# Kernel optimization log

Measured on AMD Instinct MI355X. Metric: run time of the kernel, lower is better.

## Reference

```python
import jax, jax.numpy as jnp
import numpy as np

D, H, F, E, K = 1024, 16, 2048, 8, 2
EPS = 1e-5


def layernorm(x, g, b):
    m = jnp.mean(x, axis=-1, keepdims=True)
    v = jnp.mean((x - m) ** 2, axis=-1, keepdims=True)
    return (x - m) * jax.lax.rsqrt(v + EPS) * g + b


def mha(q_in, k_in, v_in, wq, wk, wv, bq, bk, bv, wo, bo):
    B, Tq, Dm = q_in.shape
    Tk = k_in.shape[1]
    dh = Dm // H
    q = (q_in @ wq + bq).reshape(B, Tq, H, dh)
    k = (k_in @ wk + bk).reshape(B, Tk, H, dh)
    v = (v_in @ wv + bv).reshape(B, Tk, H, dh)
    scores = jnp.einsum('bqhd,bkhd->bhqk', q, k) / jnp.sqrt(jnp.asarray(dh, q.dtype))
    attn = jax.nn.softmax(scores, axis=-1)
    out = jnp.einsum('bhqk,bkhd->bqhd', attn, v).reshape(B, Tq, Dm)
    return out @ wo + bo


def moe(x, rw, rb, w1, b1, w2, b2):
    B, T, Dm = x.shape
    xt = x.reshape(-1, Dm)                      # [N, D]
    N = xt.shape[0]
    logits = xt @ rw + rb                       # [N, E]
    probs = jax.nn.softmax(logits, axis=-1)
    topv, topi = jax.lax.top_k(probs, K)        # [N, K]
    gates = topv / jnp.sum(topv, axis=-1, keepdims=True)
    dense_gates = jnp.zeros((N, E), x.dtype).at[jnp.arange(N)[:, None], topi].set(gates)
    h = jax.nn.relu(jnp.einsum('td,edf->etf', xt, w1) + b1[:, None, :])  # [E, N, F]
    y = jnp.einsum('etf,efd->etd', h, w2) + b2[:, None, :]               # [E, N, D]
    out = jnp.einsum('te,etd->td', dense_gates, y).reshape(B, T, Dm)
    frac = jnp.mean(jnp.sum(jax.nn.one_hot(topi, E, dtype=x.dtype), axis=1) / K, axis=0)  # [E]
    importance = jnp.mean(probs, axis=0)        # [E]
    lb_loss = E * jnp.sum(frac * importance)
    return out, lb_loss


def forward(tgt, memory,
            sa_wq, sa_wk, sa_wv, sa_bq, sa_bk, sa_bv, sa_wo, sa_bo,
            ca_wq, ca_wk, ca_wv, ca_bq, ca_bk, ca_bv, ca_wo, ca_bo,
            ln1_g, ln1_b, ln2_g, ln2_b, ln3_g, ln3_b,
            rw, rb, w1, b1, w2, b2):
    t2 = mha(tgt, tgt, tgt, sa_wq, sa_wk, sa_wv, sa_bq, sa_bk, sa_bv, sa_wo, sa_bo)
    t = layernorm(tgt + t2, ln1_g, ln1_b)
    t2 = mha(t, memory, memory, ca_wq, ca_wk, ca_wv, ca_bq, ca_bk, ca_bv, ca_wo, ca_bo)
    t = layernorm(t + t2, ln2_g, ln2_b)
    t2, lb = moe(t, rw, rb, w1, b1, w2, b2)
    t = layernorm(t + t2, ln3_g, ln3_b)
    return t, lb


def setup_inputs() -> dict:
    key = jax.random.key(0)
    ks = jax.random.split(key, 24)
    s = 1.0 / np.sqrt(D)
    inp = {
        'tgt': jax.random.normal(ks[0], (4, 512, D), jnp.float32),
        'memory': jax.random.normal(ks[1], (4, 512, D), jnp.float32),
    }
    names = ['sa_wq', 'sa_wk', 'sa_wv', 'sa_wo', 'ca_wq', 'ca_wk', 'ca_wv', 'ca_wo']
    for i, n in enumerate(names):
        inp[n] = jax.random.normal(ks[2 + i], (D, D), jnp.float32) * s
    for n in ['sa_bq', 'sa_bk', 'sa_bv', 'sa_bo', 'ca_bq', 'ca_bk', 'ca_bv', 'ca_bo']:
        inp[n] = jnp.zeros((D,), jnp.float32)
    for n in ['ln1_g', 'ln2_g', 'ln3_g']:
        inp[n] = jnp.ones((D,), jnp.float32)
    for n in ['ln1_b', 'ln2_b', 'ln3_b']:
        inp[n] = jnp.zeros((D,), jnp.float32)
    inp['rw'] = jax.random.normal(ks[10], (D, E), jnp.float32) * s
    inp['rb'] = jnp.zeros((E,), jnp.float32)
    inp['w1'] = jax.random.normal(ks[11], (E, D, F), jnp.float32) * s
    inp['b1'] = jnp.zeros((E, F), jnp.float32)
    inp['w2'] = jax.random.normal(ks[12], (E, F, D), jnp.float32) * (1.0 / np.sqrt(F))
    inp['b2'] = jnp.zeros((E, D), jnp.float32)
    return inp


def reference(tgt, memory,
              sa_wq, sa_wk, sa_wv, sa_bq, sa_bk, sa_bv, sa_wo, sa_bo,
              ca_wq, ca_wk, ca_wv, ca_bq, ca_bk, ca_bv, ca_wo, ca_bo,
              ln1_g, ln1_b, ln2_g, ln2_b, ln3_g, ln3_b,
              rw, rb, w1, b1, w2, b2):
    return forward(tgt, memory,
                   sa_wq, sa_wk, sa_wv, sa_bq, sa_bk, sa_bv, sa_wo, sa_bo,
                   ca_wq, ca_wk, ca_wv, ca_bq, ca_bk, ca_bv, ca_wo, ca_bo,
                   ln1_g, ln1_b, ln2_g, ln2_b, ln3_g, ln3_b,
                   rw, rb, w1, b1, w2, b2)
```

## Files before the change

kernel.cpp:

```cpp
#include <hip/hip_runtime.h>

constexpr int Dm = 1024;
constexpr int NH = 16;
constexpr int Ff = 2048;
constexpr int NE = 8;
constexpr int Bn = 4;
constexpr int Tn = 512;
constexpr int Nt = 2048;

typedef float  f32x4  __attribute__((ext_vector_type(4)));
typedef __bf16 bf16x8 __attribute__((ext_vector_type(8)));
typedef unsigned short u16x8 __attribute__((ext_vector_type(8)));

__device__ inline unsigned short f2bf(float f) {
    unsigned u = __builtin_bit_cast(unsigned, f);
    u += 0x7FFFu + ((u >> 16) & 1u);
    return (unsigned short)(u >> 16);
}
__device__ inline float bf2f(unsigned short h) {
    unsigned u = (unsigned)h << 16;
    return __builtin_bit_cast(float, u);
}
__device__ inline void splitbf(float x, unsigned short& hi, unsigned short& lo) {
    hi = f2bf(x);
    lo = f2bf(x - bf2f(hi));
}
__device__ inline bf16x8 ld_frag(const unsigned short* p) {
    return __builtin_bit_cast(bf16x8, *(const u16x8*)p);
}

template <int SPLIT, int ABF, int CBF, int ACC>
__global__ __launch_bounds__(256) void gemm_bf16_kernel(
    const void* __restrict__ Ain, int lda,
    const float* __restrict__ W0, const float* __restrict__ W1,
    const float* __restrict__ W2, int ldw, size_t weStride,
    const float* __restrict__ B0, const float* __restrict__ B1,
    const float* __restrict__ B2, size_t beStride,
    void* __restrict__ Cout, int ldc,
    int Mparam, int K,
    const int* __restrict__ lst, int lstStride, const int* __restrict__ cnt,
    int mode, int relu,
    const void* __restrict__ Ain2, const float* __restrict__ W0b,
    const float* __restrict__ W1b, const float* __restrict__ B0b,
    const float* __restrict__ B1b, void* __restrict__ Cout2, int ldc2,
    int xSplit,
    const float* __restrict__ gatep, float* __restrict__ accOut)
{
    __shared__ __align__(16) unsigned short AsH[128 * 40];
    __shared__ __align__(16) unsigned short WsH[128 * 40];
    __shared__ __align__(16) unsigned short AsL[SPLIT ? 128 * 40 : 1];
    __shared__ __align__(16) unsigned short WsL[SPLIT ? 128 * 40 : 1];
    __shared__ int inIdx[128];
    __shared__ int outIdx[128];

    const int e = blockIdx.z;
    const int M = (mode == 0) ? Mparam : cnt[e];
    const int m0 = blockIdx.y * 128;
    if (m0 >= M) return;

    int bx = blockIdx.x;
    const void* Aptr = Ain;
    void* Cptr = Cout;
    int myldc = ldc;
    const float *w0 = W0, *w1 = W1, *w2 = W2, *b0 = B0, *b1 = B1, *b2 = B2;
    if (xSplit && bx >= xSplit) {
        bx -= xSplit;
        Aptr = Ain2; Cptr = Cout2; myldc = ldc2;
        w0 = W0b; w1 = W1b; w2 = W1b; b0 = B0b; b1 = B1b; b2 = B1b;
    }
    const int n0 = bx * 128;
    const int seg = n0 >> 10;
    const float* W = ((seg == 0) ? w0 : (seg == 1) ? w1 : w2) + (size_t)e * weStride;
    const float* bias = ((seg == 0) ? b0 : (seg == 1) ? b1 : b2) + (size_t)e * beStride;
    const int nseg = n0 & 1023;
    const int tid = threadIdx.x;

    if (tid < 128) {
        int g = m0 + tid;
        bool valid = g < M;
        int gi, go;
        if (mode == 0) { gi = valid ? g : (M - 1); go = valid ? g : -1; }
        else {
            int pid = lst[(size_t)e * lstStride + (valid ? g : 0)];
            gi = (mode == 1) ? (pid >> 1) : pid;
            go = valid ? pid : -1;
        }
        inIdx[tid] = gi;
        outIdx[tid] = go;
    }
    __syncthreads();

    const int ar = tid >> 1, ahalf = tid & 1;
    const int bn = (tid & 63) * 2, bko = ((tid >> 6) & 3) * 8;
    const float* aBaseF = ABF ? nullptr
        : ((const float*)Aptr + (size_t)inIdx[ar] * lda + ahalf * 16);
    const unsigned short* aBaseB = ABF
        ? ((const unsigned short*)Aptr + (size_t)inIdx[ar] * lda + ahalf * 16)
        : nullptr;
    const float* wBase = W + (size_t)bko * ldw + nseg + bn;

    const int lane = tid & 63, wv = tid >> 6;
    const int wy = (wv >> 1) * 64, wx = (wv & 1) * 64;
    const int l15 = lane & 15, quad = lane >> 4;

    f32x4 acc[4][4];
    #pragma unroll
    for (int i = 0; i < 4; ++i)
        #pragma unroll
        for (int j = 0; j < 4; ++j) acc[i][j] = (f32x4)0.f;

    float av[16];
    u16x8 a16[2];
    float2 wreg[8];

    auto loadA = [&](int k0) {
        if (ABF) {
            const unsigned short* ap = aBaseB + k0;
            a16[0] = *(const u16x8*)(ap);
            a16[1] = *(const u16x8*)(ap + 8);
        } else {
            const float* ap = aBaseF + k0;
            *(float4*)&av[0]  = *(const float4*)(ap);
            *(float4*)&av[4]  = *(const float4*)(ap + 4);
            *(float4*)&av[8]  = *(const float4*)(ap + 8);
            *(float4*)&av[12] = *(const float4*)(ap + 12);
        }
    };
    auto loadW = [&](int k0) {
        const float* wp = wBase + (size_t)k0 * ldw;
        #pragma unroll
        for (int j = 0; j < 8; ++j) wreg[j] = *(const float2*)(wp + (size_t)j * ldw);
    };
    auto storeA = [&]() {
        if (ABF) {
            *(u16x8*)&AsH[ar * 40 + ahalf * 16]     = a16[0];
            *(u16x8*)&AsH[ar * 40 + ahalf * 16 + 8] = a16[1];
        } else {
            u16x8 h0, h1, l0, l1;
            #pragma unroll
            for (int i = 0; i < 8; ++i) {
                if (SPLIT) {
                    unsigned short hh, ll;
                    splitbf(av[i], hh, ll); h0[i] = hh; l0[i] = ll;
                    splitbf(av[8 + i], hh, ll); h1[i] = hh; l1[i] = ll;
                } else {
                    h0[i] = f2bf(av[i]);
                    h1[i] = f2bf(av[8 + i]);
                }
            }
            *(u16x8*)&AsH[ar * 40 + ahalf * 16]     = h0;
            *(u16x8*)&AsH[ar * 40 + ahalf * 16 + 8] = h1;
            if (SPLIT) {
                *(u16x8*)&AsL[ar * 40 + ahalf * 16]     = l0;
                *(u16x8*)&AsL[ar * 40 + ahalf * 16 + 8] = l1;
            }
        }
    };
    auto storeW = [&]() {
        u16x8 h0, h1, l0, l1;
        #pragma unroll
        for (int j = 0; j < 8; ++j) {
            if (SPLIT) {
                unsigned short hh, ll;
                splitbf(wreg[j].x, hh, ll); h0[j] = hh; l0[j] = ll;
                splitbf(wreg[j].y, hh, ll); h1[j] = hh; l1[j] = ll;
            } else {
                h0[j] = f2bf(wreg[j].x);
                h1[j] = f2bf(wreg[j].y);
            }
        }
        *(u16x8*)&WsH[bn * 40 + bko]       = h0;
        *(u16x8*)&WsH[(bn + 1) * 40 + bko] = h1;
        if (SPLIT) {
            *(u16x8*)&WsL[bn * 40 + bko]       = l0;
            *(u16x8*)&WsL[(bn + 1) * 40 + bko] = l1;
        }
    };

    loadA(0);
    loadW(0);
    for (int k0 = 0; k0 < K; k0 += 32) {
        storeA();
        storeW();
        __syncthreads();
        if (k0 + 32 < K) { loadA(k0 + 32); loadW(k0 + 32); }
        bf16x8 ah[4], bh[4], al[4], bl[4];
        #pragma unroll
        for (int mi = 0; mi < 4; ++mi)
            ah[mi] = ld_frag(&AsH[(wy + mi * 16 + l15) * 40 + quad * 8]);
        #pragma unroll
        for (int ni = 0; ni < 4; ++ni)
            bh[ni] = ld_frag(&WsH[(wx + ni * 16 + l15) * 40 + quad * 8]);
        if (SPLIT) {
            #pragma unroll
            for (int mi = 0; mi < 4; ++mi)
                al[mi] = ld_frag(&AsL[(wy + mi * 16 + l15) * 40 + quad * 8]);
            #pragma unroll
            for (int ni = 0; ni < 4; ++ni)
                bl[ni] = ld_frag(&WsL[(wx + ni * 16 + l15) * 40 + quad * 8]);
        }
        #pragma unroll
        for (int mi = 0; mi < 4; ++mi)
            #pragma unroll
            for (int ni = 0; ni < 4; ++ni) {
                acc[mi][ni] = __builtin_amdgcn_mfma_f32_16x16x32_bf16(
                    ah[mi], bh[ni], acc[mi][ni], 0, 0, 0);
                if (SPLIT) {
                    acc[mi][ni] = __builtin_amdgcn_mfma_f32_16x16x32_bf16(
                        ah[mi], bl[ni], acc[mi][ni], 0, 0, 0);
                    acc[mi][ni] = __builtin_amdgcn_mfma_f32_16x16x32_bf16(
                        al[mi], bh[ni], acc[mi][ni], 0, 0, 0);
                }
            }
        __syncthreads();
    }

    #pragma unroll
    for (int mi = 0; mi < 4; ++mi) {
        #pragma unroll
        for (int r = 0; r < 4; ++r) {
            int rl = wy + mi * 16 + quad * 4 + r;
            int orow = outIdx[rl];
            if (orow < 0) continue;
            #pragma unroll
            for (int ni = 0; ni < 4; ++ni) {
                int col = n0 + wx + ni * 16 + l15;
                float val = acc[mi][ni][r] + bias[col & 1023];
                if (relu) val = fmaxf(val, 0.f);
                if (ACC) {
                    float g = gatep[orow];
                    atomicAdd(&accOut[(size_t)(orow >> 1) * Dm + col], g * val);
                } else if (CBF) {
                    ((unsigned short*)Cptr)[(size_t)orow * myldc + col] = f2bf(val);
                } else {
                    ((float*)Cptr)[(size_t)orow * myldc + col] = val;
                }
            }
        }
    }
}

__global__ __launch_bounds__(256) void attn_kernel(
    const float* __restrict__ Qp, int qld,
    const float* __restrict__ Kp, int kld, int kOff,
    const float* __restrict__ Vp, int vld, int vOff,
    float* __restrict__ O)
{
    __shared__ __align__(16) unsigned short KtH[64 * 72], KtL[64 * 72];
    __shared__ __align__(16) unsigned short VtH[64 * 72], VtL[64 * 72];
    __shared__ __align__(16) unsigned short PtH[4][16 * 72], PtL[4][16 * 72];

    const int tid = threadIdx.x, lane = tid & 63, wv = tid >> 6;
    const int quad = lane >> 4, l15 = lane & 15;
    const int b = blockIdx.z, h = blockIdx.y, q0 = blockIdx.x * 64;
    const int bT = b * Tn;

    bf16x8 aqh[2], aql[2];
    {
        const float* qp = Qp + (size_t)(bT + q0 + wv * 16 + l15) * qld + h * 64;
        #pragma unroll
        for (int s = 0; s < 2; ++s) {
            float v[8];
            *(float4*)&v[0] = *(const float4*)(qp + s * 32 + quad * 8);
            *(float4*)&v[4] = *(const float4*)(qp + s * 32 + quad * 8 + 4);
            u16x8 th, tl;
            #pragma unroll
            for (int i = 0; i < 8; ++i) {
                unsigned short hh, ll;
                splitbf(v[i], hh, ll); th[i] = hh; tl[i] = ll;
            }
            aqh[s] = __builtin_bit_cast(bf16x8, th);
            aql[s] = __builtin_bit_cast(bf16x8, tl);
        }
    }

    f32x4 oacc[4];
    #pragma unroll
    for (int i = 0; i < 4; ++i) oacc[i] = (f32x4)0.f;
    float mrow[4] = {-1e30f, -1e30f, -1e30f, -1e30f};
    float lrow[4] = {0.f, 0.f, 0.f, 0.f};

    const int rr = tid >> 2, cc = tid & 3;

    float kf[16], vf[16];
    auto loadKV = [&](int kt0) {
        const float* kr = Kp + (size_t)(bT + kt0 + rr) * kld + kOff + h * 64 + cc * 16;
        *(float4*)&kf[0]  = *(const float4*)(kr);
        *(float4*)&kf[4]  = *(const float4*)(kr + 4);
        *(float4*)&kf[8]  = *(const float4*)(kr + 8);
        *(float4*)&kf[12] = *(const float4*)(kr + 12);
        const float* vr = Vp + (size_t)(bT + kt0 + rr) * vld + vOff + h * 64 + cc * 16;
        *(float4*)&vf[0]  = *(const float4*)(vr);
        *(float4*)&vf[4]  = *(const float4*)(vr + 4);
        *(float4*)&vf[8]  = *(const float4*)(vr + 8);
        *(float4*)&vf[12] = *(const float4*)(vr + 12);
    };
    auto storeKV = [&]() {
        u16x8 h0, h1, l0, l1;
        #pragma unroll
        for (int i = 0; i < 8; ++i) {
            unsigned short hh, ll;
            splitbf(kf[i], hh, ll); h0[i] = hh; l0[i] = ll;
            splitbf(kf[8 + i], hh, ll); h1[i] = hh; l1[i] = ll;
        }
        *(u16x8*)&KtH[rr * 72 + cc * 16]     = h0;
        *(u16x8*)&KtH[rr * 72 + cc * 16 + 8] = h1;
        *(u16x8*)&KtL[rr * 72 + cc * 16]     = l0;
        *(u16x8*)&KtL[rr * 72 + cc * 16 + 8] = l1;
        #pragma unroll
        for (int i = 0; i < 16; ++i) {
            unsigned short hh, ll;
            splitbf(vf[i], hh, ll);
            VtH[(cc * 16 + i) * 72 + rr] = hh;
            VtL[(cc * 16 + i) * 72 + rr] = ll;
        }
    };

    loadKV(0);
    for (int kt0 = 0; kt0 < Tn; kt0 += 64) {
        storeKV();
        __syncthreads();
        if (kt0 + 64 < Tn) loadKV(kt0 + 64);

        f32x4 sacc[4];
        #pragma unroll
        for (int nt = 0; nt < 4; ++nt) {
            sacc[nt] = (f32x4)0.f;
            #pragma unroll
            for (int s = 0; s < 2; ++s) {
                bf16x8 bkh = ld_frag(&KtH[(nt * 16 + l15) * 72 + s * 32 + quad * 8]);
                bf16x8 bkl = ld_frag(&KtL[(nt * 16 + l15) * 72 + s * 32 + quad * 8]);
                sacc[nt] = __builtin_amdgcn_mfma_f32_16x16x32_bf16(aqh[s], bkh, sacc[nt], 0, 0, 0);
                sacc[nt] = __builtin_amdgcn_mfma_f32_16x16x32_bf16(aqh[s], bkl, sacc[nt], 0, 0, 0);
                sacc[nt] = __builtin_amdgcn_mfma_f32_16x16x32_bf16(aql[s], bkh, sacc[nt], 0, 0, 0);
            }
        }
        #pragma unroll
        for (int nt = 0; nt < 4; ++nt)
            #pragma unroll
            for (int r = 0; r < 4; ++r) sacc[nt][r] *= 0.125f;

        float alpha[4], mnew[4];
        #pragma unroll
        for (int r = 0; r < 4; ++r) {
            float mx = fmaxf(fmaxf(sacc[0][r], sacc[1][r]), fmaxf(sacc[2][r], sacc[3][r]));
            #pragma unroll
            for (int msk = 1; msk < 16; msk <<= 1) mx = fmaxf(mx, __shfl_xor(mx, msk));
            mnew[r] = fmaxf(mrow[r], mx);
            alpha[r] = __expf(mrow[r] - mnew[r]);
            mrow[r] = mnew[r];
        }
        float rs[4] = {0.f, 0.f, 0.f, 0.f};
        #pragma unroll
        for (int nt = 0; nt < 4; ++nt)
            #pragma unroll
            for (int r = 0; r < 4; ++r) {
                float p = __expf(sacc[nt][r] - mnew[r]);
                sacc[nt][r] = p;
                rs[r] += p;
            }
        #pragma unroll
        for (int r = 0; r < 4; ++r) {
            #pragma unroll
            for (int msk = 1; msk < 16; msk <<= 1) rs[r] += __shfl_xor(rs[r], msk);
            lrow[r] = lrow[r] * alpha[r] + rs[r];
        }
        #pragma unroll
        for (int ni = 0; ni < 4; ++ni)
            #pragma unroll
            for (int r = 0; r < 4; ++r) oacc[ni][r] *= alpha[r];

        #pragma unroll
        for (int nt = 0; nt < 4; ++nt)
            #pragma unroll
            for (int r = 0; r < 4; ++r) {
                unsigned short hh, ll;
                splitbf(sacc[nt][r], hh, ll);
                PtH[wv][(quad * 4 + r) * 72 + nt * 16 + l15] = hh;
                PtL[wv][(quad * 4 + r) * 72 + nt * 16 + l15] = ll;
            }
        asm volatile("s_waitcnt lgkmcnt(0)" ::: "memory");

        #pragma unroll
        for (int s = 0; s < 2; ++s) {
            bf16x8 aph = ld_frag(&PtH[wv][l15 * 72 + s * 32 + quad * 8]);
            bf16x8 apl = ld_frag(&PtL[wv][l15 * 72 + s * 32 + quad * 8]);
            #pragma unroll
            for (int ni = 0; ni < 4; ++ni) {
                bf16x8 bvh = ld_frag(&VtH[(ni * 16 + l15) * 72 + s * 32 + quad * 8]);
                bf16x8 bvl = ld_frag(&VtL[(ni * 16 + l15) * 72 + s * 32 + quad * 8]);
                oacc[ni] = __builtin_amdgcn_mfma_f32_16x16x32_bf16(aph, bvh, oacc[ni], 0, 0, 0);
                oacc[ni] = __builtin_amdgcn_mfma_f32_16x16x32_bf16(aph, bvl, oacc[ni], 0, 0, 0);
                oacc[ni] = __builtin_amdgcn_mfma_f32_16x16x32_bf16(apl, bvh, oacc[ni], 0, 0, 0);
            }
        }
        __syncthreads();
    }

    #pragma unroll
    for (int r = 0; r < 4; ++r) {
        float inv = 1.f / lrow[r];
        int orow = bT + q0 + wv * 16 + quad * 4 + r;
        #pragma unroll
        for (int ni = 0; ni < 4; ++ni) {
            int col = h * 64 + ni * 16 + l15;
            O[(size_t)orow * Dm + col] = oacc[ni][r] * inv;
        }
    }
}

__global__ __launch_bounds__(256) void ln_residual_kernel(
    const float* __restrict__ X, const float* __restrict__ R,
    const float* __restrict__ g, const float* __restrict__ bta,
    float* __restrict__ Out)
{
    __shared__ float red[8];
    const int t = blockIdx.x, tid = threadIdx.x;
    float v[4];
    float s = 0.f;
    #pragma unroll
    for (int i = 0; i < 4; ++i) {
        int c = tid + i * 256;
        v[i] = X[(size_t)t * Dm + c] + R[(size_t)t * Dm + c];
        s += v[i];
    }
    #pragma unroll
    for (int off = 32; off; off >>= 1) s += __shfl_down(s, off);
    const int wid = tid >> 6;
    if ((tid & 63) == 0) red[wid] = s;
    __syncthreads();
    const float mean = (red[0] + red[1] + red[2] + red[3]) * (1.f / 1024.f);
    float s2 = 0.f;
    #pragma unroll
    for (int i = 0; i < 4; ++i) { float d = v[i] - mean; s2 += d * d; }
    #pragma unroll
    for (int off = 32; off; off >>= 1) s2 += __shfl_down(s2, off);
    if ((tid & 63) == 0) red[4 + wid] = s2;
    __syncthreads();
    const float var  = (red[4] + red[5] + red[6] + red[7]) * (1.f / 1024.f);
    const float rstd = rsqrtf(var + 1e-5f);
    #pragma unroll
    for (int i = 0; i < 4; ++i) {
        int c = tid + i * 256;
        Out[(size_t)t * Dm + c] = (v[i] - mean) * rstd * g[c] + bta[c];
    }
}

constexpr int RT_TPB = 32;
__global__ __launch_bounds__(256) void router_kernel(
    const float* __restrict__ X, const float* __restrict__ rw,
    const float* __restrict__ rb, float* __restrict__ gatep,
    int* __restrict__ elist, int* __restrict__ ecnt,
    float* __restrict__ impf, float* __restrict__ cntf)
{
    __shared__ float simp[NE];
    __shared__ int   scnt[NE];
    __shared__ int   sbase[NE];
    __shared__ int   sexp[RT_TPB][2];
    __shared__ int   spos[RT_TPB][2];

    const int tid = threadIdx.x, lane = tid & 63, wv = tid >> 6;
    if (tid < NE) { simp[tid] = 0.f; scnt[tid] = 0; }
    __syncthreads();

    const int t0 = blockIdx.x * RT_TPB;

    for (int i = 0; i < 8; ++i) {
        const int slot = wv * 8 + i;
        const int t = t0 + slot;
        float l[NE];
        #pragma unroll
        for (int e = 0; e < NE; ++e) l[e] = 0.f;
        #pragma unroll
        for (int j = 0; j < Dm / 64; ++j) {
            int d = lane + j * 64;
            float x = X[(size_t)t * Dm + d];
            #pragma unroll
            for (int e = 0; e < NE; ++e) l[e] += x * rw[d * NE + e];
        }
        #pragma unroll
        for (int e = 0; e < NE; ++e) {
            float vv = l[e];
            #pragma unroll
            for (int off = 32; off; off >>= 1) vv += __shfl_down(vv, off);
            l[e] = vv;
        }
        if (lane == 0) {
            float mx = -1e30f;
            #pragma unroll
            for (int e = 0; e < NE; ++e) { l[e] += rb[e]; mx = fmaxf(mx, l[e]); }
            float p[NE];
            float sum = 0.f;
            #pragma unroll
            for (int e = 0; e < NE; ++e) { p[e] = __expf(l[e] - mx); sum += p[e]; }
            const float inv = 1.f / sum;
            int e0 = 0, e1 = 0;
            float v0 = -1.f, v1 = -1.f;
            #pragma unroll
            for (int e = 0; e < NE; ++e) {
                float pe = p[e] * inv;
                atomicAdd(&simp[e], pe);
                if (pe > v0)      { v1 = v0; e1 = e0; v0 = pe; e0 = e; }
                else if (pe > v1) { v1 = pe; e1 = e; }
            }
            const float gs = 1.f / (v0 + v1);
            sexp[slot][0] = e0;
            sexp[slot][1] = e1;
            spos[slot][0] = atomicAdd(&scnt[e0], 1);
            spos[slot][1] = atomicAdd(&scnt[e1], 1);
            gatep[2 * t]     = v0 * gs;
            gatep[2 * t + 1] = v1 * gs;
        }
    }
    __syncthreads();

    if (tid < NE) {
        sbase[tid] = atomicAdd(&ecnt[tid], scnt[tid]);
        atomicAdd(&impf[tid], simp[tid]);
        atomicAdd(&cntf[tid], (float)scnt[tid]);
    }
    __syncthreads();

    if (tid < RT_TPB * 2) {
        const int slot = tid >> 1, k = tid & 1;
        const int e = sexp[slot][k];
        elist[e * Nt + sbase[e] + spos[slot][k]] = 2 * (t0 + slot) + k;
    }
}

__global__ __launch_bounds__(256) void zero_kernel(
    float* __restrict__ t2, int* __restrict__ ecnt,
    float* __restrict__ impf, float* __restrict__ cntf)
{
    int i = blockIdx.x * 256 + threadIdx.x;
    *(float4*)&t2[(size_t)i * 4] = make_float4(0.f, 0.f, 0.f, 0.f);
    if (blockIdx.x == 0 && threadIdx.x < NE) {
        ecnt[threadIdx.x] = 0;
        impf[threadIdx.x] = 0.f;
        cntf[threadIdx.x] = 0.f;
    }
}

__global__ void lb_kernel(const float* __restrict__ impf,
                          const float* __restrict__ cntf,
                          float* __restrict__ out)
{
    if (threadIdx.x == 0) {
        float s = 0.f;
        for (int e = 0; e < NE; ++e) s += cntf[e] * impf[e];
        out[0] = (float)NE * s / ((float)Nt * 2.f * (float)Nt);
    }
}

extern "C" void kernel_launch(void* const* d_in, const int* in_sizes, int n_in,
                              void* d_out, int out_size, void* d_ws, size_t ws_size,
                              hipStream_t stream)
{
    const float* tgt   = (const float*)d_in[0];
    const float* memry = (const float*)d_in[1];
    const float* sa_wq = (const float*)d_in[2];
    const float* sa_wk = (const float*)d_in[3];
    const float* sa_wv = (const float*)d_in[4];
    const float* sa_wo = (const float*)d_in[5];
    const float* ca_wq = (const float*)d_in[6];
    const float* ca_wk = (const float*)d_in[7];
    const float* ca_wv = (const float*)d_in[8];
    const float* ca_wo = (const float*)d_in[9];
    const float* sa_bq = (const float*)d_in[10];
    const float* sa_bk = (const float*)d_in[11];
    const float* sa_bv = (const float*)d_in[12];
    const float* sa_bo = (const float*)d_in[13];
    const float* ca_bq = (const float*)d_in[14];
    const float* ca_bk = (const float*)d_in[15];
    const float* ca_bv = (const float*)d_in[16];
    const float* ca_bo = (const float*)d_in[17];
    const float* ln1_g = (const float*)d_in[18];
    const float* ln2_g = (const float*)d_in[19];
    const float* ln3_g = (const float*)d_in[20];
    const float* ln1_b = (const float*)d_in[21];
    const float* ln2_b = (const float*)d_in[22];
    const float* ln3_b = (const float*)d_in[23];
    const float* rw    = (const float*)d_in[24];
    const float* rb    = (const float*)d_in[25];
    const float* w1    = (const float*)d_in[26];
    const float* b1    = (const float*)d_in[27];
    const float* w2    = (const float*)d_in[28];
    const float* b2    = (const float*)d_in[29];

    float* ws = (float*)d_ws;
    const size_t ND = (size_t)Nt * Dm;
    float* qkv  = ws;
    float* qc   = ws;
    unsigned short* hbuf16 = (unsigned short*)ws;
    float* attnO = ws + 3 * ND;
    float* t2   = ws + 4 * ND;
    float* tb   = ws + 5 * ND;
    float* kvc  = ws + 6 * ND;
    float* gatep = ws + 8 * ND;
    int*   elist = (int*)(gatep + 2 * Nt);
    int*   ecnt  = elist + NE * Nt;
    float* impf  = (float*)(ecnt + NE);
    float* cntf  = impf + NE;
    float* outp  = (float*)d_out;

    dim3 blk(256);
    dim3 attnGrid(Tn / 64, NH, Bn);

    gemm_bf16_kernel<1, 0, 0, 0><<<dim3(40, 16, 1), blk, 0, stream>>>(
        tgt, Dm, sa_wq, sa_wk, sa_wv, Dm, 0, sa_bq, sa_bk, sa_bv, 0,
        qkv, 3 * Dm, Nt, Dm, nullptr, 0, nullptr, 0, 0,
        memry, ca_wk, ca_wv, ca_bk, ca_bv, kvc, 2 * Dm, 24,
        nullptr, nullptr);
    attn_kernel<<<attnGrid, blk, 0, stream>>>(
        qkv, 3 * Dm, qkv, 3 * Dm, 1024, qkv, 3 * Dm, 2048, attnO);
    gemm_bf16_kernel<1, 0, 0, 0><<<dim3(8, 16, 1), blk, 0, stream>>>(
        attnO, Dm, sa_wo, sa_wo, sa_wo, Dm, 0, sa_bo, sa_bo, sa_bo, 0,
        t2, Dm, Nt, Dm, nullptr, 0, nullptr, 0, 0,
        nullptr, nullptr, nullptr, nullptr, nullptr, nullptr, 0, 0,
        nullptr, nullptr);
    ln_residual_kernel<<<Nt, blk, 0, stream>>>(tgt, t2, ln1_g, ln1_b, tb);

    gemm_bf16_kernel<1, 0, 0, 0><<<dim3(8, 16, 1), blk, 0, stream>>>(
        tb, Dm, ca_wq, ca_wq, ca_wq, Dm, 0, ca_bq, ca_bq, ca_bq, 0,
        qc, Dm, Nt, Dm, nullptr, 0, nullptr, 0, 0,
        nullptr, nullptr, nullptr, nullptr, nullptr, nullptr, 0, 0,
        nullptr, nullptr);
    attn_kernel<<<attnGrid, blk, 0, stream>>>(
        qc, Dm, kvc, 2 * Dm, 0, kvc, 2 * Dm, 1024, attnO);
    gemm_bf16_kernel<1, 0, 0, 0><<<dim3(8, 16, 1), blk, 0, stream>>>(
        attnO, Dm, ca_wo, ca_wo, ca_wo, Dm, 0, ca_bo, ca_bo, ca_bo, 0,
        t2, Dm, Nt, Dm, nullptr, 0, nullptr, 0, 0,
        nullptr, nullptr, nullptr, nullptr, nullptr, nullptr, 0, 0,
        nullptr, nullptr);
    ln_residual_kernel<<<Nt, blk, 0, stream>>>(tb, t2, ln2_g, ln2_b, tb);

    zero_kernel<<<(Nt * Dm) / 1024, blk, 0, stream>>>(t2, ecnt, impf, cntf);
    router_kernel<<<Nt / RT_TPB, blk, 0, stream>>>(tb, rw, rb, gatep, elist, ecnt, impf, cntf);
    gemm_bf16_kernel<0, 0, 1, 0><<<dim3(16, 16, 8), blk, 0, stream>>>(
        tb, Dm, w1, w1 + 1024, w1 + 1024, Ff, (size_t)Dm * Ff, b1, b1 + 1024, b1 + 1024, Ff,
        hbuf16, Ff, 0, Dm, elist, Nt, ecnt, 1, 1,
        nullptr, nullptr, nullptr, nullptr, nullptr, nullptr, 0, 0,
        nullptr, nullptr);
    gemm_bf16_kernel<0, 1, 0, 1><<<dim3(8, 16, 8), blk, 0, stream>>>(
        hbuf16, Ff, w2, w2, w2, Dm, (size_t)Ff * Dm, b2, b2, b2, Dm,
        nullptr, Dm, 0, Ff, elist, Nt, ecnt, 2, 0,
        nullptr, nullptr, nullptr, nullptr, nullptr, nullptr, 0, 0,
        gatep, t2);
    ln_residual_kernel<<<Nt, blk, 0, stream>>>(tb, t2, ln3_g, ln3_b, outp);
    lb_kernel<<<1, 64, 0, stream>>>(impf, cntf, outp + ND);
}
```

Before: 819.6 us.

## Halve GEMM M-tile to 64 and drop register prefetch in GEMM and attention

The GEMM block tile shrinks from 128 to 64 rows, with each wave now computing a 32x64 sub-tile, and grids double along y to give more blocks. The register double-buffering (load the next tile before the MFMA loop) is removed from both the GEMM and attention kernels, so loads go straight to shared memory each iteration. This lowers register and shared-memory use per block, which should raise occupancy and parallelism. The cost is less overlap between global loads and compute, and more weight-tile reloading across blocks.

```diff
diff --git a/kernel.cpp b/kernel.cpp
--- a/kernel.cpp
+++ b/kernel.cpp
@@ -46,16 +46,16 @@
     int xSplit,
     const float* __restrict__ gatep, float* __restrict__ accOut)
 {
-    __shared__ __align__(16) unsigned short AsH[128 * 40];
+    __shared__ __align__(16) unsigned short AsH[64 * 40];
     __shared__ __align__(16) unsigned short WsH[128 * 40];
-    __shared__ __align__(16) unsigned short AsL[SPLIT ? 128 * 40 : 1];
+    __shared__ __align__(16) unsigned short AsL[SPLIT ? 64 * 40 : 1];
     __shared__ __align__(16) unsigned short WsL[SPLIT ? 128 * 40 : 1];
-    __shared__ int inIdx[128];
-    __shared__ int outIdx[128];
+    __shared__ int inIdx[64];
+    __shared__ int outIdx[64];
 
     const int e = blockIdx.z;
     const int M = (mode == 0) ? Mparam : cnt[e];
-    const int m0 = blockIdx.y * 128;
+    const int m0 = blockIdx.y * 64;
     if (m0 >= M) return;
 
     int bx = blockIdx.x;
@@ -75,7 +75,7 @@
     const int nseg = n0 & 1023;
     const int tid = threadIdx.x;
 
-    if (tid < 128) {
+    if (tid < 64) {
         int g = m0 + tid;
         bool valid = g < M;
         int gi, go;
@@ -90,117 +90,89 @@
     }
     __syncthreads();
 
-    const int ar = tid >> 1, ahalf = tid & 1;
+    const int ar = tid >> 2, ahalf = tid & 3;
     const int bn = (tid & 63) * 2, bko = ((tid >> 6) & 3) * 8;
     const float* aBaseF = ABF ? nullptr
-        : ((const float*)Aptr + (size_t)inIdx[ar] * lda + ahalf * 16);
+        : ((const float*)Aptr + (size_t)inIdx[ar] * lda + ahalf * 8);
     const unsigned short* aBaseB = ABF
-        ? ((const unsigned short*)Aptr + (size_t)inIdx[ar] * lda + ahalf * 16)
+        ? ((const unsigned short*)Aptr + (size_t)inIdx[ar] * lda + ahalf * 8)
         : nullptr;
     const float* wBase = W + (size_t)bko * ldw + nseg + bn;
 
     const int lane = tid & 63, wv = tid >> 6;
-    const int wy = (wv >> 1) * 64, wx = (wv & 1) * 64;
+    const int wy = (wv >> 1) * 32, wx = (wv & 1) * 64;
     const int l15 = lane & 15, quad = lane >> 4;
 
-    f32x4 acc[4][4];
-    #pragma unroll
-    for (int i = 0; i < 4; ++i)
+    f32x4 acc[2][4];
+    #pragma unroll
+    for (int i = 0; i < 2; ++i)
         #pragma unroll
         for (int j = 0; j < 4; ++j) acc[i][j] = (f32x4)0.f;
 
-    float av[16];
-    u16x8 a16[2];
-    float2 wreg[8];
-
-    auto loadA = [&](int k0) {
+    for (int k0 = 0; k0 < K; k0 += 32) {
         if (ABF) {
             const unsigned short* ap = aBaseB + k0;
-            a16[0] = *(const u16x8*)(ap);
-            a16[1] = *(const u16x8*)(ap + 8);
+            *(u16x8*)&AsH[ar * 40 + ahalf * 8] = *(const u16x8*)(ap);
         } else {
             const float* ap = aBaseF + k0;
-            *(float4*)&av[0]  = *(const float4*)(ap);
-            *(float4*)&av[4]  = *(const float4*)(ap + 4);
-            *(float4*)&av[8]  = *(const float4*)(ap + 8);
-            *(float4*)&av[12] = *(const float4*)(ap + 12);
-        }
-    };
-    auto loadW = [&](int k0) {
-        const float* wp = wBase + (size_t)k0 * ldw;
-        #pragma unroll
-        for (int j = 0; j < 8; ++j) wreg[j] = *(const float2*)(wp + (size_t)j * ldw);
-    };
-    auto storeA = [&]() {
-        if (ABF) {
-            *(u16x8*)&AsH[ar * 40 + ahalf * 16]     = a16[0];
-            *(u16x8*)&AsH[ar * 40 + ahalf * 16 + 8] = a16[1];
-        } else {
-            u16x8 h0, h1, l0, l1;
+            float v[8];
+            *(float4*)&v[0] = *(const float4*)(ap);
+            *(float4*)&v[4] = *(const float4*)(ap + 4);
+            u16x8 h0, l0;
             #pragma unroll
             for (int i = 0; i < 8; ++i) {
                 if (SPLIT) {
                     unsigned short hh, ll;
-                    splitbf(av[i], hh, ll); h0[i] = hh; l0[i] = ll;
-                    splitbf(av[8 + i], hh, ll); h1[i] = hh; l1[i] = ll;
+                    splitbf(v[i], hh, ll); h0[i] = hh; l0[i] = ll;
                 } else {
-                    h0[i] = f2bf(av[i]);
-                    h1[i] = f2bf(av[8 + i]);
+                    h0[i] = f2bf(v[i]);
                 }
             }
-            *(u16x8*)&AsH[ar * 40 + ahalf * 16]     = h0;
-            *(u16x8*)&AsH[ar * 40 + ahalf * 16 + 8] = h1;
+            *(u16x8*)&AsH[ar * 40 + ahalf * 8] = h0;
+            if (SPLIT) *(u16x8*)&AsL[ar * 40 + ahalf * 8] = l0;
+        }
+        {
+            const float* wp = wBase + (size_t)k0 * ldw;
+            float2 wr[8];
+            #pragma unroll
+            for (int j = 0; j < 8; ++j) wr[j] = *(const float2*)(wp + (size_t)j * ldw);
+            u16x8 h0, h1, l0, l1;
+            #pragma unroll
+            for (int j = 0; j < 8; ++j) {
+                if (SPLIT) {
+                    unsigned short hh, ll;
+                    splitbf(wr[j].x, hh, ll); h0[j] = hh; l0[j] = ll;
+                    splitbf(wr[j].y, hh, ll); h1[j] = hh; l1[j] = ll;
+                } else {
+                    h0[j] = f2bf(wr[j].x);
+                    h1[j] = f2bf(wr[j].y);
+                }
+            }
+            *(u16x8*)&WsH[bn * 40 + bko]       = h0;
+            *(u16x8*)&WsH[(bn + 1) * 40 + bko] = h1;
             if (SPLIT) {
-                *(u16x8*)&AsL[ar * 40 + ahalf * 16]     = l0;
-                *(u16x8*)&AsL[ar * 40 + ahalf * 16 + 8] = l1;
-            }
-        }
-    };
-    auto storeW = [&]() {
-        u16x8 h0, h1, l0, l1;
-        #pragma unroll
-        for (int j = 0; j < 8; ++j) {
-            if (SPLIT) {
-                unsigned short hh, ll;
-                splitbf(wreg[j].x, hh, ll); h0[j] = hh; l0[j] = ll;
-                splitbf(wreg[j].y, hh, ll); h1[j] = hh; l1[j] = ll;
-            } else {
-                h0[j] = f2bf(wreg[j].x);
-                h1[j] = f2bf(wreg[j].y);
-            }
-        }
-        *(u16x8*)&WsH[bn * 40 + bko]       = h0;
-        *(u16x8*)&WsH[(bn + 1) * 40 + bko] = h1;
-        if (SPLIT) {
-            *(u16x8*)&WsL[bn * 40 + bko]       = l0;
-            *(u16x8*)&WsL[(bn + 1) * 40 + bko] = l1;
-        }
-    };
-
-    loadA(0);
-    loadW(0);
-    for (int k0 = 0; k0 < K; k0 += 32) {
-        storeA();
-        storeW();
+                *(u16x8*)&WsL[bn * 40 + bko]       = l0;
+                *(u16x8*)&WsL[(bn + 1) * 40 + bko] = l1;
+            }
+        }
         __syncthreads();
-        if (k0 + 32 < K) { loadA(k0 + 32); loadW(k0 + 32); }
-        bf16x8 ah[4], bh[4], al[4], bl[4];
-        #pragma unroll
-        for (int mi = 0; mi < 4; ++mi)
+        bf16x8 ah[2], bh[4], al[2], bl[4];
+        #pragma unroll
+        for (int mi = 0; mi < 2; ++mi)
             ah[mi] = ld_frag(&AsH[(wy + mi * 16 + l15) * 40 + quad * 8]);
         #pragma unroll
         for (int ni = 0; ni < 4; ++ni)
             bh[ni] = ld_frag(&WsH[(wx + ni * 16 + l15) * 40 + quad * 8]);
         if (SPLIT) {
             #pragma unroll
-            for (int mi = 0; mi < 4; ++mi)
+            for (int mi = 0; mi < 2; ++mi)
                 al[mi] = ld_frag(&AsL[(wy + mi * 16 + l15) * 40 + quad * 8]);
             #pragma unroll
             for (int ni = 0; ni < 4; ++ni)
                 bl[ni] = ld_frag(&WsL[(wx + ni * 16 + l15) * 40 + quad * 8]);
         }
         #pragma unroll
-        for (int mi = 0; mi < 4; ++mi)
+        for (int mi = 0; mi < 2; ++mi)
             #pragma unroll
             for (int ni = 0; ni < 4; ++ni) {
                 acc[mi][ni] = __builtin_amdgcn_mfma_f32_16x16x32_bf16(
@@ -216,7 +188,7 @@
     }
 
     #pragma unroll
-    for (int mi = 0; mi < 4; ++mi) {
+    for (int mi = 0; mi < 2; ++mi) {
         #pragma unroll
         for (int r = 0; r < 4; ++r) {
             int rl = wy + mi * 16 + quad * 4 + r;
@@ -282,45 +254,41 @@
 
     const int rr = tid >> 2, cc = tid & 3;
 
-    float kf[16], vf[16];
-    auto loadKV = [&](int kt0) {
-        const float* kr = Kp + (size_t)(bT + kt0 + rr) * kld + kOff + h * 64 + cc * 16;
-        *(float4*)&kf[0]  = *(const float4*)(kr);
-        *(float4*)&kf[4]  = *(const float4*)(kr + 4);
-        *(float4*)&kf[8]  = *(const float4*)(kr + 8);
-        *(float4*)&kf[12] = *(const float4*)(kr + 12);
-        const float* vr = Vp + (size_t)(bT + kt0 + rr) * vld + vOff + h * 64 + cc * 16;
-        *(float4*)&vf[0]  = *(const float4*)(vr);
-        *(float4*)&vf[4]  = *(const float4*)(vr + 4);
-        *(float4*)&vf[8]  = *(const float4*)(vr + 8);
-        *(float4*)&vf[12] = *(const float4*)(vr + 12);
-    };
-    auto storeKV = [&]() {
-        u16x8 h0, h1, l0, l1;
-        #pragma unroll
-        for (int i = 0; i < 8; ++i) {
-            unsigned short hh, ll;
-            splitbf(kf[i], hh, ll); h0[i] = hh; l0[i] = ll;
-            splitbf(kf[8 + i], hh, ll); h1[i] = hh; l1[i] = ll;
-        }
-        *(u16x8*)&KtH[rr * 72 + cc * 16]     = h0;
-        *(u16x8*)&KtH[rr * 72 + cc * 16 + 8] = h1;
-        *(u16x8*)&KtL[rr * 72 + cc * 16]     = l0;
-        *(u16x8*)&KtL[rr * 72 + cc * 16 + 8] = l1;
-        #pragma unroll
-        for (int i = 0; i < 16; ++i) {
-            unsigned short hh, ll;
-            splitbf(vf[i], hh, ll);
-            VtH[(cc * 16 + i) * 72 + rr] = hh;
-            VtL[(cc * 16 + i) * 72 + rr] = ll;
-        }
-    };
-
-    loadKV(0);
     for (int kt0 = 0; kt0 < Tn; kt0 += 64) {
-        storeKV();
+        {
+            const float* kr = Kp + (size_t)(bT + kt0 + rr) * kld + kOff + h * 64 + cc * 16;
+            float v[16];
+            *(float4*)&v[0]  = *(const float4*)(kr);
+            *(float4*)&v[4]  = *(const float4*)(kr + 4);
+            *(float4*)&v[8]  = *(const float4*)(kr + 8);
+            *(float4*)&v[12] = *(const float4*)(kr + 12);
+            u16x8 h0, h1, l0, l1;
+            #pragma unroll
+            for (int i = 0; i < 8; ++i) {
+                unsigned short hh, ll;
+                splitbf(v[i], hh, ll); h0[i] = hh; l0[i] = ll;
+                splitbf(v[8 + i], hh, ll); h1[i] = hh; l1[i] = ll;
+            }
+            *(u16x8*)&KtH[rr * 72 + cc * 16]     = h0;
+            *(u16x8*)&KtH[rr * 72 + cc * 16 + 8] = h1;
+            *(u16x8*)&KtL[rr * 72 + cc * 16]     = l0;
+            *(u16x8*)&KtL[rr * 72 + cc * 16 + 8] = l1;
+
+            const float* vr = Vp + (size_t)(bT + kt0 + rr) * vld + vOff + h * 64 + cc * 16;
+            float fv[16];
+            *(float4*)&fv[0]  = *(const float4*)(vr);
+            *(float4*)&fv[4]  = *(const float4*)(vr + 4);
+            *(float4*)&fv[8]  = *(const float4*)(vr + 8);
+            *(float4*)&fv[12] = *(const float4*)(vr + 12);
+            #pragma unroll
+            for (int i = 0; i < 16; ++i) {
+                unsigned short hh, ll;
+                splitbf(fv[i], hh, ll);
+                VtH[(cc * 16 + i) * 72 + rr] = hh;
+                VtL[(cc * 16 + i) * 72 + rr] = ll;
+            }
+        }
         __syncthreads();
-        if (kt0 + 64 < Tn) loadKV(kt0 + 64);
 
         f32x4 sacc[4];
         #pragma unroll
@@ -606,28 +574,28 @@
     dim3 blk(256);
     dim3 attnGrid(Tn / 64, NH, Bn);
 
-    gemm_bf16_kernel<1, 0, 0, 0><<<dim3(40, 16, 1), blk, 0, stream>>>(
+    gemm_bf16_kernel<1, 0, 0, 0><<<dim3(40, 32, 1), blk, 0, stream>>>(
         tgt, Dm, sa_wq, sa_wk, sa_wv, Dm, 0, sa_bq, sa_bk, sa_bv, 0,
         qkv, 3 * Dm, Nt, Dm, nullptr, 0, nullptr, 0, 0,
         memry, ca_wk, ca_wv, ca_bk, ca_bv, kvc, 2 * Dm, 24,
         nullptr, nullptr);
     attn_kernel<<<attnGrid, blk, 0, stream>>>(
         qkv, 3 * Dm, qkv, 3 * Dm, 1024, qkv, 3 * Dm, 2048, attnO);
-    gemm_bf16_kernel<1, 0, 0, 0><<<dim3(8, 16, 1), blk, 0, stream>>>(
+    gemm_bf16_kernel<1, 0, 0, 0><<<dim3(8, 32, 1), blk, 0, stream>>>(
         attnO, Dm, sa_wo, sa_wo, sa_wo, Dm, 0, sa_bo, sa_bo, sa_bo, 0,
         t2, Dm, Nt, Dm, nullptr, 0, nullptr, 0, 0,
         nullptr, nullptr, nullptr, nullptr, nullptr, nullptr, 0, 0,
         nullptr, nullptr);
     ln_residual_kernel<<<Nt, blk, 0, stream>>>(tgt, t2, ln1_g, ln1_b, tb);
 
-    gemm_bf16_kernel<1, 0, 0, 0><<<dim3(8, 16, 1), blk, 0, stream>>>(
+    gemm_bf16_kernel<1, 0, 0, 0><<<dim3(8, 32, 1), blk, 0, stream>>>(
         tb, Dm, ca_wq, ca_wq, ca_wq, Dm, 0, ca_bq, ca_bq, ca_bq, 0,
         qc, Dm, Nt, Dm, nullptr, 0, nullptr, 0, 0,
         nullptr, nullptr, nullptr, nullptr, nullptr, nullptr, 0, 0,
         nullptr, nullptr);
     attn_kernel<<<attnGrid, blk, 0, stream>>>(
         qc, Dm, kvc, 2 * Dm, 0, kvc, 2 * Dm, 1024, attnO);
-    gemm_bf16_kernel<1, 0, 0, 0><<<dim3(8, 16, 1), blk, 0, stream>>>(
+    gemm_bf16_kernel<1, 0, 0, 0><<<dim3(8, 32, 1), blk, 0, stream>>>(
         attnO, Dm, ca_wo, ca_wo, ca_wo, Dm, 0, ca_bo, ca_bo, ca_bo, 0,
         t2, Dm, Nt, Dm, nullptr, 0, nullptr, 0, 0,
         nullptr, nullptr, nullptr, nullptr, nullptr, nullptr, 0, 0,
@@ -636,12 +604,12 @@
 
     zero_kernel<<<(Nt * Dm) / 1024, blk, 0, stream>>>(t2, ecnt, impf, cntf);
     router_kernel<<<Nt / RT_TPB, blk, 0, stream>>>(tb, rw, rb, gatep, elist, ecnt, impf, cntf);
-    gemm_bf16_kernel<0, 0, 1, 0><<<dim3(16, 16, 8), blk, 0, stream>>>(
+    gemm_bf16_kernel<0, 0, 1, 0><<<dim3(16, 32, 8), blk, 0, stream>>>(
         tb, Dm, w1, w1 + 1024, w1 + 1024, Ff, (size_t)Dm * Ff, b1, b1 + 1024, b1 + 1024, Ff,
         hbuf16, Ff, 0, Dm, elist, Nt, ecnt, 1, 1,
         nullptr, nullptr, nullptr, nullptr, nullptr, nullptr, 0, 0,
         nullptr, nullptr);
-    gemm_bf16_kernel<0, 1, 0, 1><<<dim3(8, 16, 8), blk, 0, stream>>>(
+    gemm_bf16_kernel<0, 1, 0, 1><<<dim3(8, 32, 8), blk, 0, stream>>>(
         hbuf16, Ff, w2, w2, w2, Dm, (size_t)Ff * Dm, b2, b2, b2, Dm,
         nullptr, Dm, 0, Ff, elist, Nt, ecnt, 2, 0,
         nullptr, nullptr, nullptr, nullptr, nullptr, nullptr, 0, 0,
```

After: 825.8 us. Within noise of the previous version (+0.8%).
